# Optimization experiments

Measured on AMD Instinct MI355X. Metric: run time of the kernel, lower is better.

## Reference

```python
import jax, jax.numpy as jnp
import numpy as np

BETA = 0.9       # membrane decay
THR = 1.0        # snntorch Leaky default threshold
SLOPE = 25.0     # fast_sigmoid surrogate slope (forward-only here)


def _heaviside(x):
    return (x > 0).astype(x.dtype)


def setup_inputs() -> dict:
    key = jax.random.key(0)
    ks = jax.random.split(key, 4)
    B, D, H1, H2, C = 4096, 1024, 2048, 1024, 64
    x = jax.random.normal(ks[0], (B, D), jnp.float32)
    W1 = jax.random.normal(ks[1], (H1, D), jnp.float32) * 0.02
    b1 = jnp.zeros((H1,), jnp.float32)
    W2 = jax.random.normal(ks[2], (H2, H1), jnp.float32) * 0.02
    b2 = jnp.zeros((H2,), jnp.float32)
    Wo = jax.random.normal(ks[3], (C, H2), jnp.float32) * 0.02
    bo = jnp.zeros((C,), jnp.float32)
    return {"x": x, "W1": W1, "b1": b1, "W2": W2, "b2": b2,
            "Wo": Wo, "bo": bo, "num_steps": 20}


def reference(x, W1, b1, W2, b2, Wo, bo, num_steps):
    B = x.shape[0]
    mem1 = jnp.zeros((B, W1.shape[0]), x.dtype)
    mem2 = jnp.zeros((B, W2.shape[0]), x.dtype)
    spk_sum = jnp.zeros((B, W2.shape[0]), x.dtype)

    def step(carry, _):
        cur, m1, m2, ss = carry
        # Layer 1: Linear + Leaky (reset-by-subtraction, persistent mem)
        h1 = cur @ W1.T + b1                      # [B, H1]
        r1 = _heaviside(m1 - THR)                 # reset from previous mem
        m1 = BETA * m1 + h1 - r1 * THR
        s1 = _heaviside(m1 - THR)
        # Layer 2: Linear + Leaky
        h2 = s1 @ W2.T + b2                       # [B, H2]
        r2 = _heaviside(m2 - THR)
        m2 = BETA * m2 + h2 - r2 * THR
        s2 = _heaviside(m2 - THR)
        # NOTE: s2 feeds back into layer-1 Linear next step (cur = x only at t=0)
        return (s2, m1, m2, ss + s2), None

    (cur, mem1, mem2, spk_sum), _ = jax.lax.scan(
        step, (x, mem1, mem2, spk_sum), None, length=num_steps)
    return (spk_sum / num_steps) @ Wo.T + bo
```

## Files before the change

### kernel.cpp

```cpp
#include <hip/hip_runtime.h>
#include <hip/hip_bf16.h>

#define B_   4096
#define D_   1024
#define H1_  2048
#define H2_  1024
#define C_   64

typedef double d4 __attribute__((ext_vector_type(4)));

#if defined(__has_builtin)
#  if __has_builtin(__builtin_amdgcn_mfma_f64_16x16x4f64)
#    define MFMA64(A, B, C) __builtin_amdgcn_mfma_f64_16x16x4f64((A), (B), (C), 0, 0, 0)
#    define HAVE_MFMA64 1
#  elif __has_builtin(__builtin_amdgcn_mfma_f64_16x16x4_f64)
#    define MFMA64(A, B, C) __builtin_amdgcn_mfma_f64_16x16x4_f64((A), (B), (C), 0, 0, 0)
#    define HAVE_MFMA64 1
#  endif
#endif

__global__ void k_probe(int* flag) {
#if defined(HAVE_MFMA64)
    int lane = threadIdx.x & 63;
    int lr = lane & 15, lk = lane >> 4;
    double a  = (double)(5 * lr + 3 * lk + 1);
    double bb = (double)(11 * lk + 2 * lr + 2);
    d4 c = {0.0, 0.0, 0.0, 0.0};
    c = MFMA64(a, bb, c);
    int okm[4] = {1, 1, 1, 1};
#pragma unroll
    for (int j = 0; j < 4; ++j) {
        double e1 = 0, e2 = 0, e3 = 0, e4 = 0;
        for (int k = 0; k < 4; ++k) {
            e1 += (double)(5 * (4 * lk + j) + 3 * k + 1) * (double)(11 * k + 2 * lr + 2);
            e2 += (double)(5 * lr + 3 * k + 1) * (double)(11 * k + 2 * (4 * lk + j) + 2);
            e3 += (double)(5 * (lk + 4 * j) + 3 * k + 1) * (double)(11 * k + 2 * lr + 2);
            e4 += (double)(5 * lr + 3 * k + 1) * (double)(11 * k + 2 * (lk + 4 * j) + 2);
        }
        if (c[j] != e1) okm[0] = 0;
        if (c[j] != e2) okm[1] = 0;
        if (c[j] != e3) okm[2] = 0;
        if (c[j] != e4) okm[3] = 0;
    }
    int f = 0;
    for (int m = 3; m >= 0; --m) {
        unsigned long long all = __ballot(okm[m] != 0);
        if (all == ~0ULL) f = m + 1;
    }
    if (lane == 0) flag[0] = f;
#else
    if ((threadIdx.x & 63) == 0) flag[0] = 0;
#endif
}

__global__ __launch_bounds__(256) void k_transpose(const float* __restrict__ in,
                                                   float* __restrict__ out,
                                                   int R, int C) {
    __shared__ float t[32][33];
    int c0 = blockIdx.x * 32;
    int r0 = blockIdx.y * 32;
    int lx = threadIdx.x;
    int ly = threadIdx.y;
#pragma unroll
    for (int q = 0; q < 4; ++q) {
        int rr = ly + 8 * q;
        t[rr][lx] = in[(size_t)(r0 + rr) * C + (c0 + lx)];
    }
    __syncthreads();
#pragma unroll
    for (int q = 0; q < 4; ++q) {
        int cc = ly + 8 * q;
        out[(size_t)(c0 + cc) * R + (r0 + lx)] = t[lx][cc];
    }
}

#define GBM 128
#define GBN 128
#define GBK 16
#define AIDXSZ 2208
#define AIDX(k, r) ((k) * 136 + (((k) >> 2) << 3) + (r))
__global__ __launch_bounds__(512, 4) void k_gemm_mfma(const float* __restrict__ x,
                                                      const float* __restrict__ W1,
                                                      const float* __restrict__ b1,
                                                      double* __restrict__ m1out,
                                                      const int* __restrict__ flag) {
#if defined(HAVE_MFMA64)
    int fm = flag[0];
    if (fm < 1 || fm > 4) return;
    __shared__ float As[AIDXSZ];
    __shared__ float Bs[AIDXSZ];

    int tid = threadIdx.x;
    int m0 = blockIdx.x * GBM;
    int n0 = blockIdx.y * GBN;
    int w = tid >> 6, lane = tid & 63;
    int wr = w >> 2;
    int wc = w & 3;
    int lr = lane & 15, lk = lane >> 4;
    int srow = tid >> 2;
    int g    = tid & 3;
    int skq  = g * 4;
    int sbase = AIDX(skq, srow);

    d4 acc[4][2];
#pragma unroll
    for (int i = 0; i < 4; ++i)
#pragma unroll
        for (int j = 0; j < 2; ++j) acc[i][j] = (d4){0.0, 0.0, 0.0, 0.0};

    for (int k0 = 0; k0 < D_; k0 += GBK) {
        float4 av = *(const float4*)&x [(size_t)(m0 + srow) * D_ + k0 + skq];
        float4 bv = *(const float4*)&W1[(size_t)(n0 + srow) * D_ + k0 + skq];
        __syncthreads();
        As[sbase + 0 * 136] = av.x;
        As[sbase + 1 * 136] = av.y;
        As[sbase + 2 * 136] = av.z;
        As[sbase + 3 * 136] = av.w;
        Bs[sbase + 0 * 136] = bv.x;
        Bs[sbase + 1 * 136] = bv.y;
        Bs[sbase + 2 * 136] = bv.z;
        Bs[sbase + 3 * 136] = bv.w;
        __syncthreads();
#pragma unroll
        for (int kb = 0; kb < 4; ++kb) {
            int abase = AIDX(kb * 4 + lk, wr * 64 + lr);
            int bbase = AIDX(kb * 4 + lk, wc * 32 + lr);
            double a[4], bfr[2];
#pragma unroll
            for (int i = 0; i < 4; ++i)
                a[i] = (double)As[abase + 16 * i];
#pragma unroll
            for (int j = 0; j < 2; ++j)
                bfr[j] = (double)Bs[bbase + 16 * j];
#pragma unroll
            for (int i = 0; i < 4; ++i)
#pragma unroll
                for (int j = 0; j < 2; ++j)
                    acc[i][j] = MFMA64(a[i], bfr[j], acc[i][j]);
        }
    }
#pragma unroll
    for (int j = 0; j < 2; ++j)
#pragma unroll
        for (int i = 0; i < 4; ++i)
#pragma unroll
            for (int r = 0; r < 4; ++r) {
                int rin = (fm == 1) ? (4 * lk + r) : (fm == 2) ? lr
                        : (fm == 3) ? (lk + 4 * r) : lr;
                int cin = (fm == 1) ? lr : (fm == 2) ? (4 * lk + r)
                        : (fm == 3) ? lr : (lk + 4 * r);
                int row = m0 + wr * 64 + 16 * i + rin;
                int col = n0 + wc * 32 + 16 * j + cin;
                m1out[(size_t)row * H1_ + col] = acc[i][j][r] + (double)b1[col];
            }
#else
    (void)x; (void)W1; (void)b1; (void)m1out; (void)flag;
#endif
}

#define BM 128
#define BN 128
#define BK 8
__global__ __launch_bounds__(256) void k_gemm1(const float* __restrict__ x,
                                               const float* __restrict__ W1,
                                               const float* __restrict__ b1,
                                               double* __restrict__ m1out,
                                               const int* __restrict__ flag) {
    int fm = flag[0];
    if (fm >= 1 && fm <= 4) return;
    __shared__ double As[BK][BM + 4];
    __shared__ double Bs[BK][BN + 4];

    int tid = threadIdx.x;
    int m0 = blockIdx.x * BM;
    int n0 = blockIdx.y * BN;
    int tx = tid & 15;
    int ty = tid >> 4;
    int lr = tid >> 1;
    int lk = (tid & 1) * 4;

    double acc[8][8] = {};

    for (int k0 = 0; k0 < D_; k0 += BK) {
        float4 av = *(const float4*)&x [(size_t)(m0 + lr) * D_ + k0 + lk];
        float4 bv = *(const float4*)&W1[(size_t)(n0 + lr) * D_ + k0 + lk];
        __syncthreads();
        As[lk + 0][lr] = (double)av.x;
        As[lk + 1][lr] = (double)av.y;
        As[lk + 2][lr] = (double)av.z;
        As[lk + 3][lr] = (double)av.w;
        Bs[lk + 0][lr] = (double)bv.x;
        Bs[lk + 1][lr] = (double)bv.y;
        Bs[lk + 2][lr] = (double)bv.z;
        Bs[lk + 3][lr] = (double)bv.w;
        __syncthreads();
#pragma unroll
        for (int kk = 0; kk < BK; ++kk) {
            double a[8], b[8];
#pragma unroll
            for (int i = 0; i < 8; ++i) a[i] = As[kk][tx + 16 * i];
#pragma unroll
            for (int j = 0; j < 8; ++j) b[j] = Bs[kk][ty + 16 * j];
#pragma unroll
            for (int i = 0; i < 8; ++i)
#pragma unroll
                for (int j = 0; j < 8; ++j)
                    acc[i][j] += a[i] * b[j];
        }
    }
#pragma unroll
    for (int j = 0; j < 8; ++j) {
        double bj = (double)b1[n0 + ty + 16 * j];
#pragma unroll
        for (int i = 0; i < 8; ++i) {
            m1out[(size_t)(m0 + tx + 16 * i) * H1_ + (n0 + ty + 16 * j)] =
                acc[i][j] + bj;
        }
    }
}

__global__ __launch_bounds__(256) void k_snn(const double* __restrict__ m1_0,
                                             const float* __restrict__ b1,
                                             const float* __restrict__ W1T,
                                             const float* __restrict__ W2T,
                                             const float* __restrict__ b2,
                                             const float* __restrict__ Wo,
                                             const float* __restrict__ bo,
                                             const int* __restrict__ nsteps_p,
                                             float* __restrict__ out) {
    __shared__ __align__(16) double pjbuf[H2_];
    __shared__ __align__(16) int l2idx[H2_];
    __shared__ unsigned long long s1by[32];
    __shared__ unsigned long long s2nb[32];
    __shared__ int ncnt[2];
    __shared__ int anyb1[4], anyb2[4];

    int* l1idx = (int*)pjbuf;

    int b = blockIdx.x;
    int tid = threadIdx.x;
    int lane = tid & 63;
    int wv = tid >> 6;
    int T = nsteps_p[0];

    double m1r[8], m2r[4];
    float b1f[8], b2f[4];
    int cnt[4];

    const double* m1p = m1_0 + (size_t)b * H1_ + 8 * tid;
    {
        double2 v0 = *(const double2*)(m1p + 0);
        double2 v1 = *(const double2*)(m1p + 2);
        double2 v2 = *(const double2*)(m1p + 4);
        double2 v3 = *(const double2*)(m1p + 6);
        m1r[0] = v0.x; m1r[1] = v0.y; m1r[2] = v1.x; m1r[3] = v1.y;
        m1r[4] = v2.x; m1r[5] = v2.y; m1r[6] = v3.x; m1r[7] = v3.y;
    }
    {
        float4 f0 = *(const float4*)(b1 + 8 * tid);
        float4 f1 = *(const float4*)(b1 + 8 * tid + 4);
        b1f[0] = f0.x; b1f[1] = f0.y; b1f[2] = f0.z; b1f[3] = f0.w;
        b1f[4] = f1.x; b1f[5] = f1.y; b1f[6] = f1.z; b1f[7] = f1.w;
        float4 f2 = *(const float4*)(b2 + 4 * tid);
        b2f[0] = f2.x; b2f[1] = f2.y; b2f[2] = f2.z; b2f[3] = f2.w;
    }
#pragma unroll
    for (int q = 0; q < 4; ++q) { m2r[q] = 0.0; cnt[q] = 0; }

    int anyS2 = 0;

#define ACC2(v) { m2r[0] += (double)(v).x; m2r[1] += (double)(v).y; \
                  m2r[2] += (double)(v).z; m2r[3] += (double)(v).w; }

    for (int t = 0; t < T; ++t) {
        if (t > 0) {
#pragma unroll
            for (int q = 0; q < 8; ++q)
                m1r[q] = 0.9 * m1r[q] - (m1r[q] > 1.0 ? 1.0 : 0.0) + (double)b1f[q];
            if (anyS2) {
                int n2 = ncnt[1];
                const char* Wc = (const char*)W1T;
                size_t toff = (size_t)tid << 5;
                for (int k2 = 0; k2 < n2; ++k2) {
                    const float4* c4 = (const float4*)(Wc + l2idx[k2] + toff);
                    float4 va = c4[0];
                    float4 vb = c4[1];
                    m1r[0] += (double)va.x; m1r[1] += (double)va.y;
                    m1r[2] += (double)va.z; m1r[3] += (double)va.w;
                    m1r[4] += (double)vb.x; m1r[5] += (double)vb.y;
                    m1r[6] += (double)vb.z; m1r[7] += (double)vb.w;
                }
            }
        }
        unsigned bflag = 0;
#pragma unroll
        for (int q = 0; q < 8; ++q) bflag |= (m1r[q] > 1.0 ? 1u : 0u) << q;
        ((unsigned char*)s1by)[tid] = (unsigned char)bflag;
        {
            int wa = __any((int)bflag);
            if (lane == 0) anyb1[wv] = wa;
        }
#pragma unroll
        for (int q = 0; q < 4; ++q)
            m2r[q] = 0.9 * m2r[q] - (m2r[q] > 1.0 ? 1.0 : 0.0) + (double)b2f[q];
        {
            unsigned nib = 0;
#pragma unroll
            for (int q = 0; q < 4; ++q) nib |= (m2r[q] > 1.0 ? 1u : 0u) << q;
            ((unsigned char*)s2nb)[tid] = (unsigned char)nib;
            int wa = __any((int)nib);
            if (lane == 0) anyb2[wv] = wa;
        }
        __syncthreads();
        int any1 = anyb1[0] | anyb1[1] | anyb1[2] | anyb1[3];
        if (any1) {
            if (tid < 64) {
                unsigned long long bits = (tid < 32) ? s1by[tid] : 0ULL;
                int pc = __popcll(bits);
                int sc = pc;
#pragma unroll
                for (int d = 1; d < 64; d <<= 1) {
                    int o = __shfl_up(sc, d);
                    if (tid >= d) sc += o;
                }
                if (tid == 63) ncnt[0] = sc;
                int off = sc - pc;
                int base = tid << 6;
                while (bits) {
                    l1idx[off++] = (base + __builtin_ctzll(bits)) << 12;
                    bits &= bits - 1;
                }
            }
            __syncthreads();
            {
                int n1 = ncnt[0];
                const char* Wc = (const char*)W2T;
                size_t toff = (size_t)tid << 4;
                int k = 0;
                for (; k + 8 <= n1; k += 8) {
                    int4 oa = *(const int4*)&l1idx[k];
                    int4 ob = *(const int4*)&l1idx[k + 4];
                    float4 v0 = *(const float4*)(Wc + oa.x + toff);
                    float4 v1 = *(const float4*)(Wc + oa.y + toff);
                    float4 v2 = *(const float4*)(Wc + oa.z + toff);
                    float4 v3 = *(const float4*)(Wc + oa.w + toff);
                    float4 v4 = *(const float4*)(Wc + ob.x + toff);
                    float4 v5 = *(const float4*)(Wc + ob.y + toff);
                    float4 v6 = *(const float4*)(Wc + ob.z + toff);
                    float4 v7 = *(const float4*)(Wc + ob.w + toff);
                    ACC2(v0); ACC2(v1); ACC2(v2); ACC2(v3);
                    ACC2(v4); ACC2(v5); ACC2(v6); ACC2(v7);
                }
                for (; k < n1; ++k) {
                    float4 v = *(const float4*)(Wc + l1idx[k] + toff);
                    ACC2(v);
                }
            }
            {
                unsigned nib = 0;
#pragma unroll
                for (int q = 0; q < 4; ++q) nib |= (m2r[q] > 1.0 ? 1u : 0u) << q;
                ((unsigned char*)s2nb)[tid] = (unsigned char)nib;
                int wa = __any((int)nib);
                if (lane == 0) anyb2[wv] = wa;
            }
            __syncthreads();
        }
        anyS2 = anyb2[0] | anyb2[1] | anyb2[2] | anyb2[3];
#pragma unroll
        for (int q = 0; q < 4; ++q) cnt[q] += (m2r[q] > 1.0) ? 1 : 0;
        if (anyS2) {
            if (tid < 64) {
                unsigned long long wbits = 0ULL;
                if (tid < 16) {
                    unsigned long long w0 = s2nb[2 * tid];
                    unsigned long long w1 = s2nb[2 * tid + 1];
                    w0 &= 0x0F0F0F0F0F0F0F0FULL;
                    w0 = (w0 | (w0 >> 4)) & 0x00FF00FF00FF00FFULL;
                    w0 = (w0 | (w0 >> 8)) & 0x0000FFFF0000FFFFULL;
                    w0 = (w0 | (w0 >> 16)) & 0x00000000FFFFFFFFULL;
                    w1 &= 0x0F0F0F0F0F0F0F0FULL;
                    w1 = (w1 | (w1 >> 4)) & 0x00FF00FF00FF00FFULL;
                    w1 = (w1 | (w1 >> 8)) & 0x0000FFFF0000FFFFULL;
                    w1 = (w1 | (w1 >> 16)) & 0x00000000FFFFFFFFULL;
                    wbits = w0 | (w1 << 32);
                }
                int pc = __popcll(wbits);
                int sc = pc;
#pragma unroll
                for (int d = 1; d < 64; d <<= 1) {
                    int o = __shfl_up(sc, d);
                    if (tid >= d) sc += o;
                }
                if (tid == 63) ncnt[1] = sc;
                int off = sc - pc;
                int base = tid << 6;
                while (wbits) {
                    l2idx[off++] = (base + __builtin_ctzll(wbits)) << 13;
                    wbits &= wbits - 1;
                }
            }
            __syncthreads();
        }
    }
#undef ACC2

    __syncthreads();
#pragma unroll
    for (int q = 0; q < 4; ++q)
        pjbuf[4 * tid + q] = (double)cnt[q] / (double)T;
    {
        unsigned nib = 0;
#pragma unroll
        for (int q = 0; q < 4; ++q) nib |= (cnt[q] > 0 ? 1u : 0u) << q;
        ((unsigned char*)s2nb)[tid] = (unsigned char)nib;
    }
    __syncthreads();
    if (tid < 64) {
        unsigned long long wbits = 0ULL;
        if (tid < 16) {
            unsigned long long w0 = s2nb[2 * tid];
            unsigned long long w1 = s2nb[2 * tid + 1];
            w0 &= 0x0F0F0F0F0F0F0F0FULL;
            w0 = (w0 | (w0 >> 4)) & 0x00FF00FF00FF00FFULL;
            w0 = (w0 | (w0 >> 8)) & 0x0000FFFF0000FFFFULL;
            w0 = (w0 | (w0 >> 16)) & 0x00000000FFFFFFFFULL;
            w1 &= 0x0F0F0F0F0F0F0F0FULL;
            w1 = (w1 | (w1 >> 4)) & 0x00FF00FF00FF00FFULL;
            w1 = (w1 | (w1 >> 8)) & 0x0000FFFF0000FFFFULL;
            w1 = (w1 | (w1 >> 16)) & 0x00000000FFFFFFFFULL;
            wbits = w0 | (w1 << 32);
        }
        int pc = __popcll(wbits);
        int sc = pc;
#pragma unroll
        for (int d = 1; d < 64; d <<= 1) {
            int o = __shfl_up(sc, d);
            if (tid >= d) sc += o;
        }
        if (tid == 63) ncnt[1] = sc;
        int off = sc - pc;
        int base = tid << 6;
        while (wbits) {
            l2idx[off++] = base + __builtin_ctzll(wbits);
            wbits &= wbits - 1;
        }
    }
    __syncthreads();
    if (tid < C_) {
        int c = tid;
        int na = ncnt[1];
        const float* worow = &Wo[(size_t)c * H2_];
        double acc = 0.0;
        for (int k = 0; k < na; ++k) {
            int j = l2idx[k];
            acc += pjbuf[j] * (double)worow[j];
        }
        out[(size_t)b * C_ + c] = (float)(acc + (double)bo[c]);
    }
}

extern "C" void kernel_launch(void* const* d_in, const int* in_sizes, int n_in,
                              void* d_out, int out_size, void* d_ws, size_t ws_size,
                              hipStream_t stream) {
    const float* x  = (const float*)d_in[0];
    const float* W1 = (const float*)d_in[1];
    const float* b1 = (const float*)d_in[2];
    const float* W2 = (const float*)d_in[3];
    const float* b2 = (const float*)d_in[4];
    const float* Wo = (const float*)d_in[5];
    const float* bo = (const float*)d_in[6];
    const int* nst  = (const int*)d_in[7];
    float* out = (float*)d_out;

    size_t off_m1   = 0;
    size_t off_w1t  = off_m1 + (size_t)B_ * H1_ * 8;
    size_t off_w2t  = off_w1t + (size_t)D_ * H1_ * 4;
    size_t off_flag = off_w2t + (size_t)H1_ * H2_ * 4;
    size_t need     = off_flag + 64;
    if (ws_size < need) return;

    double* m1ws = (double*)((char*)d_ws + off_m1);
    float*  W1T  = (float*)((char*)d_ws + off_w1t);
    float*  W2T  = (float*)((char*)d_ws + off_w2t);
    int*    flag = (int*)((char*)d_ws + off_flag);

    k_probe<<<1, 64, 0, stream>>>(flag);

    k_transpose<<<dim3(D_ / 32, H1_ / 32), dim3(32, 8), 0, stream>>>(W1, W1T, H1_, D_);
    k_transpose<<<dim3(H1_ / 32, H2_ / 32), dim3(32, 8), 0, stream>>>(W2, W2T, H2_, H1_);

    k_gemm_mfma<<<dim3(B_ / GBM, H1_ / GBN), 512, 0, stream>>>(x, W1, b1, m1ws, flag);
    k_gemm1<<<dim3(B_ / BM, H1_ / BN), 256, 0, stream>>>(x, W1, b1, m1ws, flag);

    k_snn<<<B_, 256, 0, stream>>>(m1ws, b1, W1T, W2T, b2, Wo, bo, nst, out);
}
```

Baseline: 440.5 us.

## Double-buffer shared tiles in first-layer FP64 MFMA GEMM and re-pad LDS layout

Splits the shared-memory A/B tiles into two buffers so that the next K-slice's global loads are issued before the MFMA work on the current slice and written to the other buffer afterwards, cutting the loop from two barriers per iteration to one. It also changes the LDS index function to add extra per-row padding, which spreads the scattered stores and fragment reads across more banks. This doubles LDS use per block, which could limit occupancy at the declared launch bounds, and keeps the prefetched values live in registers across the MFMA loop.

```diff
diff --git a/kernel.cpp b/kernel.cpp
--- a/kernel.cpp
+++ b/kernel.cpp
@@ -77,8 +77,10 @@
 #define GBM 128
 #define GBN 128
 #define GBK 16
-#define AIDXSZ 2208
-#define AIDX(k, r) ((k) * 136 + (((k) >> 2) << 3) + (r))
+#define ABUFSZ 2320
+__device__ __forceinline__ int AIDX(int k, int r) {
+    return k * 136 + ((k >> 2) * 40) + ((k & 3) * 8) + (((k >> 1) & 1) * 8) + r;
+}
 __global__ __launch_bounds__(512, 4) void k_gemm_mfma(const float* __restrict__ x,
                                                       const float* __restrict__ W1,
                                                       const float* __restrict__ b1,
@@ -87,8 +89,8 @@
 #if defined(HAVE_MFMA64)
     int fm = flag[0];
     if (fm < 1 || fm > 4) return;
-    __shared__ float As[AIDXSZ];
-    __shared__ float Bs[AIDXSZ];
+    __shared__ float As[2][ABUFSZ];
+    __shared__ float Bs[2][ABUFSZ];
 
     int tid = threadIdx.x;
     int m0 = blockIdx.x * GBM;
@@ -100,7 +102,10 @@
     int srow = tid >> 2;
     int g    = tid & 3;
     int skq  = g * 4;
-    int sbase = AIDX(skq, srow);
+    int woff0 = AIDX(skq + 0, srow);
+    int woff1 = AIDX(skq + 1, srow);
+    int woff2 = AIDX(skq + 2, srow);
+    int woff3 = AIDX(skq + 3, srow);
 
     d4 acc[4][2];
 #pragma unroll
@@ -108,19 +113,28 @@
 #pragma unroll
         for (int j = 0; j < 2; ++j) acc[i][j] = (d4){0.0, 0.0, 0.0, 0.0};
 
-    for (int k0 = 0; k0 < D_; k0 += GBK) {
-        float4 av = *(const float4*)&x [(size_t)(m0 + srow) * D_ + k0 + skq];
-        float4 bv = *(const float4*)&W1[(size_t)(n0 + srow) * D_ + k0 + skq];
-        __syncthreads();
-        As[sbase + 0 * 136] = av.x;
-        As[sbase + 1 * 136] = av.y;
-        As[sbase + 2 * 136] = av.z;
-        As[sbase + 3 * 136] = av.w;
-        Bs[sbase + 0 * 136] = bv.x;
-        Bs[sbase + 1 * 136] = bv.y;
-        Bs[sbase + 2 * 136] = bv.z;
-        Bs[sbase + 3 * 136] = bv.w;
-        __syncthreads();
+    {
+        float4 av = *(const float4*)&x [(size_t)(m0 + srow) * D_ + skq];
+        float4 bv = *(const float4*)&W1[(size_t)(n0 + srow) * D_ + skq];
+        As[0][woff0] = av.x; As[0][woff1] = av.y;
+        As[0][woff2] = av.z; As[0][woff3] = av.w;
+        Bs[0][woff0] = bv.x; Bs[0][woff1] = bv.y;
+        Bs[0][woff2] = bv.z; Bs[0][woff3] = bv.w;
+    }
+    __syncthreads();
+
+    int cur = 0;
+    const int NT = D_ / GBK;
+    for (int t = 0; t < NT; ++t) {
+        float4 avn, bvn;
+        bool more = (t + 1 < NT);
+        if (more) {
+            int k0 = (t + 1) * GBK;
+            avn = *(const float4*)&x [(size_t)(m0 + srow) * D_ + k0 + skq];
+            bvn = *(const float4*)&W1[(size_t)(n0 + srow) * D_ + k0 + skq];
+        }
+        const float* Ac = As[cur];
+        const float* Bc = Bs[cur];
 #pragma unroll
         for (int kb = 0; kb < 4; ++kb) {
             int abase = AIDX(kb * 4 + lk, wr * 64 + lr);
@@ -128,17 +142,28 @@
             double a[4], bfr[2];
 #pragma unroll
             for (int i = 0; i < 4; ++i)
-                a[i] = (double)As[abase + 16 * i];
+                a[i] = (double)Ac[abase + 16 * i];
 #pragma unroll
             for (int j = 0; j < 2; ++j)
-                bfr[j] = (double)Bs[bbase + 16 * j];
+                bfr[j] = (double)Bc[bbase + 16 * j];
 #pragma unroll
             for (int i = 0; i < 4; ++i)
 #pragma unroll
                 for (int j = 0; j < 2; ++j)
                     acc[i][j] = MFMA64(a[i], bfr[j], acc[i][j]);
         }
-    }
+        if (more) {
+            float* An = As[cur ^ 1];
+            float* Bn = Bs[cur ^ 1];
+            An[woff0] = avn.x; An[woff1] = avn.y;
+            An[woff2] = avn.z; An[woff3] = avn.w;
+            Bn[woff0] = bvn.x; Bn[woff1] = bvn.y;
+            Bn[woff2] = bvn.z; Bn[woff3] = bvn.w;
+        }
+        __syncthreads();
+        cur ^= 1;
+    }
+
 #pragma unroll
     for (int j = 0; j < 2; ++j)
 #pragma unroll
```

Measured after the change: 446.6 us. No clear change (+1.4%).
